# Kernel optimization log

Hardware: AMD Instinct MI355X
Metric: run time of the kernel (lower is better)

Reference implementation:

```python
import jax, jax.numpy as jnp
import numpy as np

EPS = 1e-5


def _interp_conv(x, pos_in, pos_out, idx, w1, b1, w2, b2, kernel, bias):
    # x: [B, Cin, Nin]; idx: [Nout, K] neighbor indices into the input grid.
    off = pos_in[idx] - pos_out[:, None, :]            # [Nout, K, 2] relative offsets
    h = jax.nn.relu(off @ w1 + b1)                     # [Nout, K, 16] weight-net hidden
    A = h @ w2 + b2                                    # [Nout, K, T] interp weights onto T kernel taps
    feat = x[:, :, idx]                                # [B, Cin, Nout, K] irregular gather
    taps = jnp.einsum('bcnk,nkt->bcnt', feat, A)       # resample neighbors onto canonical taps
    return jnp.einsum('bcnt,oct->bon', taps, kernel) + bias[None, :, None]


def _bn_relu(x, g, b):
    # BatchNorm1d (training-style batch stats over (B, N)) + ReLU
    m = x.mean(axis=(0, 2), keepdims=True)
    v = x.var(axis=(0, 2), keepdims=True)
    return jax.nn.relu((x - m) * jax.lax.rsqrt(v + EPS) * g[None, :, None] + b[None, :, None])


def setup_inputs():
    key = jax.random.key(0)
    ks = jax.random.split(key, 24)
    B, N1, N2, N3, K, T = 16, 50176, 12544, 3136, 9, 9
    d = {}
    d['x'] = jax.random.normal(ks[0], (B, 3, N1), jnp.float32)
    d['l1'] = jax.random.uniform(ks[1], (N1, 2), jnp.float32)
    d['l2'] = jax.random.uniform(ks[2], (N2, 2), jnp.float32)
    d['l3'] = jax.random.uniform(ks[3], (N3, 2), jnp.float32)
    d['knn1'] = jax.random.randint(ks[4], (N2, K), 0, N1)
    d['knn2'] = jax.random.randint(ks[5], (N2, K), 0, N2)
    d['knn3'] = jax.random.randint(ks[6], (N2, K), 0, N2)
    d['pool_idx'] = jax.random.randint(ks[7], (N3, 4), 0, N2)
    cins = {'c1': 3, 'c2': 32, 'c3': 32}
    couts = {'c1': 32, 'c2': 32, 'c3': 64}
    for i, p in enumerate(['c1', 'c2', 'c3']):
        d[p + '_wn_w1'] = jax.random.normal(ks[8 + 4 * i], (2, 16), jnp.float32) * 0.5
        d[p + '_wn_b1'] = jnp.zeros(16, jnp.float32)
        d[p + '_wn_w2'] = jax.random.normal(ks[9 + 4 * i], (16, T), jnp.float32) * 0.3
        d[p + '_wn_b2'] = jnp.zeros(T, jnp.float32)
        d[p + '_kernel'] = jax.random.normal(ks[10 + 4 * i], (couts[p], cins[p], T), jnp.float32) * np.float32(1.0 / np.sqrt(cins[p] * T))
        d[p + '_bias'] = jnp.zeros(couts[p], jnp.float32)
    for p, c in [('bn1', 32), ('bn2', 32), ('bn3', 64)]:
        d[p + '_g'] = jnp.ones(c, jnp.float32)
        d[p + '_b'] = jnp.zeros(c, jnp.float32)
    return d


def reference(x, l1, l2, l3, knn1, knn2, knn3, pool_idx,
              c1_wn_w1, c1_wn_b1, c1_wn_w2, c1_wn_b2, c1_kernel, c1_bias,
              c2_wn_w1, c2_wn_b1, c2_wn_w2, c2_wn_b2, c2_kernel, c2_bias,
              c3_wn_w1, c3_wn_b1, c3_wn_w2, c3_wn_b2, c3_kernel, c3_bias,
              bn1_g, bn1_b, bn2_g, bn2_b, bn3_g, bn3_b):
    h = _interp_conv(x, l1, l2, knn1, c1_wn_w1, c1_wn_b1, c1_wn_w2, c1_wn_b2, c1_kernel, c1_bias)
    h = _bn_relu(h, bn1_g, bn1_b)
    h = _interp_conv(h, l2, l2, knn2, c2_wn_w1, c2_wn_b1, c2_wn_w2, c2_wn_b2, c2_kernel, c2_bias)
    h = _bn_relu(h, bn2_g, bn2_b)
    h = _interp_conv(h, l2, l2, knn3, c3_wn_w1, c3_wn_b1, c3_wn_w2, c3_wn_b2, c3_kernel, c3_bias)
    h = _bn_relu(h, bn3_g, bn3_b)
    # MaxPoolNG: max over 4 nearest neighbors on the non-uniform grid -> [B, 64, N3]
    return h[:, :, pool_idx].max(axis=-1)
```

## Files before the change

kernel.cpp:

```cpp
#include <hip/hip_runtime.h>
#include <hip/hip_bf16.h>
#include <cfloat>

#define N1C 50176
#define N2C 12544
#define N3C 3136

typedef __attribute__((ext_vector_type(8))) short short8v;
typedef __attribute__((ext_vector_type(4))) float f32x4;

static __device__ __forceinline__ unsigned short f2bf(float f){
  __hip_bfloat16 h = __float2bfloat16(f);
  return *reinterpret_cast<unsigned short*>(&h);
}
static __device__ __forceinline__ float bflo(unsigned v){
  return __uint_as_float(v << 16);
}
static __device__ __forceinline__ float bfhi(unsigned v){
  return __uint_as_float(v & 0xFFFF0000u);
}
static __device__ __forceinline__ float bf2f(unsigned short u){
  return __uint_as_float(((unsigned)u) << 16);
}
static __device__ __forceinline__ unsigned pk2(float a, float b){
  return (unsigned)f2bf(a) | ((unsigned)f2bf(b) << 16);
}

__global__ __launch_bounds__(256) void transpose_x_kernel(
    const float* __restrict__ x, unsigned short* __restrict__ xTb)
{
  __shared__ float tile[48][65];
  int n0 = blockIdx.x * 64;
  int tid = threadIdx.x;
  int i = tid & 63;
  for (int rr = tid >> 6; rr < 48; rr += 4)
    tile[rr][i] = x[(size_t)rr * N1C + n0 + i];
  __syncthreads();
  for (int j = tid; j < 64*64; j += 256){
    int ii = j >> 6, bc = j & 63, b = bc >> 2, c = bc & 3;
    float v = (c < 3) ? tile[b*3 + c][ii] : 0.f;
    xTb[(size_t)n0 * 64 + j] = f2bf(v);
  }
}

__global__ __launch_bounds__(256) void compute_A_kernel(
    const float* __restrict__ pos_in, const float* __restrict__ pos_out,
    const int* __restrict__ idx,
    const float* __restrict__ w1, const float* __restrict__ b1,
    const float* __restrict__ w2, const float* __restrict__ b2,
    float* __restrict__ Abuf)
{
  int g = blockIdx.x * 256 + threadIdx.x;
  if (g >= N2C * 9) return;
  int n = g / 9;
  int p = idx[g];
  float o0 = pos_in[2*p]   - pos_out[2*n];
  float o1 = pos_in[2*p+1] - pos_out[2*n+1];
  float A[9];
  #pragma unroll
  for (int t = 0; t < 9; t++) A[t] = b2[t];
  #pragma unroll
  for (int j = 0; j < 16; j++){
    float h = fmaxf(fmaf(o0, w1[j], fmaf(o1, w1[16+j], b1[j])), 0.f);
    #pragma unroll
    for (int t = 0; t < 9; t++) A[t] = fmaf(h, w2[j*9 + t], A[t]);
  }
  #pragma unroll
  for (int t = 0; t < 9; t++) Abuf[(size_t)g*9 + t] = A[t];
}

__global__ __launch_bounds__(256) void wcvt_kernel(
    const float* __restrict__ W, unsigned short* __restrict__ Wb,
    int total, int K, int KW, int mode)
{
  int i = blockIdx.x * 256 + threadIdx.x;
  if (i >= total) return;
  int o = i / KW, r = i % KW;
  float v;
  if (mode == 0){
    v = (r < K) ? W[o*K + r] : 0.f;
  } else {
    int t = r >> 5, c = r & 31;
    v = W[o*288 + c*9 + t];
  }
  Wb[i] = f2bf(v);
}

template<int CIN, int CINP, int COUT, int NPB, bool AFFINE>
__global__ __launch_bounds__(256) void conv_mfma_kernel(
    const unsigned short* __restrict__ in, const int* __restrict__ idx,
    const float* __restrict__ Abuf, const unsigned short* __restrict__ Wb,
    const float* __restrict__ bias,
    const float* __restrict__ scale, const float* __restrict__ shift,
    unsigned short* __restrict__ out, float* __restrict__ gpart)
{
  constexpr int K    = CIN * 9;
  constexpr int KW   = (K < 32) ? 32 : K;
  constexpr int KROW = (K < 32) ? 48 : 296;
  constexpr int CHUNKS = KW / 32;
  constexpr int OT   = COUT / 16;
  constexpr int HP   = CINP / 2;
  constexpr int PPT  = 16 * HP;

  __shared__ alignas(16) unsigned short Tb[NPB * 16 * KROW];
  __shared__ float As[NPB * 81];
  __shared__ int   Ip[NPB * 9];
  __shared__ float Sw[4 * COUT];
  __shared__ float Sq[4 * COUT];

  int n0 = blockIdx.x * NPB;
  int tid = threadIdx.x;
  for (int i = tid; i < NPB*81; i += 256) As[i] = Abuf[(size_t)n0*81 + i];
  if (tid < NPB*9) Ip[tid] = idx[n0*9 + tid];
  for (int i = tid; i < 4*COUT; i += 256){ Sw[i] = 0.f; Sq[i] = 0.f; }
  if (K < 32){
    for (int i = tid; i < NPB*16*KROW/2; i += 256) ((unsigned*)Tb)[i] = 0u;
  }
  __syncthreads();

  for (int u = tid; u < NPB*PPT; u += 256){
    int ni = u / PPT, loc = u % PPT;
    int b = loc / HP, c2 = loc % HP;
    const float* As_n = As + ni*81;
    const int*   ip   = Ip + ni*9;
    float scx=1.f, shx=0.f, scy=1.f, shy=0.f;
    if (AFFINE){
      scx = scale[2*c2];   shx = shift[2*c2];
      scy = scale[2*c2+1]; shy = shift[2*c2+1];
    }
    float fx[9], fy[9];
    #pragma unroll
    for (int k = 0; k < 9; k++){
      unsigned v = *(const unsigned*)(in + ((size_t)ip[k]*16 + b)*CINP + 2*c2);
      float x0 = bflo(v), y0 = bfhi(v);
      if (AFFINE){
        x0 = fmaxf(fmaf(x0, scx, shx), 0.f);
        y0 = fmaxf(fmaf(y0, scy, shy), 0.f);
      }
      fx[k] = x0; fy[k] = y0;
    }
    unsigned short e[18];
    #pragma unroll
    for (int t = 0; t < 9; t++){
      float s0 = 0.f, s1 = 0.f;
      #pragma unroll
      for (int k = 0; k < 9; k++){
        float a = As_n[k*9 + t];
        s0 = fmaf(fx[k], a, s0);
        s1 = fmaf(fy[k], a, s1);
      }
      e[t] = f2bf(s0); e[9+t] = f2bf(s1);
    }
    unsigned* dst = (unsigned*)(Tb + (ni*16 + b)*KROW + 18*c2);
    #pragma unroll
    for (int j = 0; j < 9; j++) dst[j] = (unsigned)e[2*j] | ((unsigned)e[2*j+1] << 16);
  }
  __syncthreads();

  int w = tid >> 6, l = tid & 63, lr = l & 15, lg = l >> 4;
  float smr[4] = {0,0,0,0}, sqr[4] = {0,0,0,0};
  int oBase = 0;
  for (int wi = w; wi < NPB*OT; wi += 4){
    int ni = wi / OT, ot = wi % OT;
    oBase = 16*ot + 4*lg;
    f32x4 acc;
    #pragma unroll
    for (int r = 0; r < 4; r++) acc[r] = bias[oBase + r];
    const short8v* ap = (const short8v*)(Wb + (size_t)(16*ot + lr)*KW) + lg;
    const short8v* bp = (const short8v*)(Tb + (ni*16 + lr)*KROW) + lg;
    #pragma unroll
    for (int kk = 0; kk < CHUNKS; kk++)
      acc = __builtin_amdgcn_mfma_f32_16x16x32_bf16(ap[kk*4], bp[kk*4], acc, 0, 0, 0);
    ushort4 o4;
    o4.x = f2bf(acc[0]); o4.y = f2bf(acc[1]); o4.z = f2bf(acc[2]); o4.w = f2bf(acc[3]);
    *(ushort4*)(out + ((size_t)(n0 + ni)*16 + lr)*COUT + oBase) = o4;
    #pragma unroll
    for (int r = 0; r < 4; r++){
      smr[r] += acc[r];
      sqr[r] = fmaf(acc[r], acc[r], sqr[r]);
    }
  }
  #pragma unroll
  for (int m = 1; m < 16; m <<= 1){
    #pragma unroll
    for (int r = 0; r < 4; r++){
      smr[r] += __shfl_xor(smr[r], m);
      sqr[r] += __shfl_xor(sqr[r], m);
    }
  }
  if (lr == 0){
    #pragma unroll
    for (int r = 0; r < 4; r++){
      Sw[w*COUT + oBase + r] = smr[r];
      Sq[w*COUT + oBase + r] = sqr[r];
    }
  }
  __syncthreads();
  for (int o = tid; o < COUT; o += 256){
    float sm = Sw[o] + Sw[COUT + o] + Sw[2*COUT + o] + Sw[3*COUT + o];
    float sq = Sq[o] + Sq[COUT + o] + Sq[2*COUT + o] + Sq[3*COUT + o];
    gpart[(size_t)blockIdx.x * 2*COUT + o] = sm;
    gpart[(size_t)blockIdx.x * 2*COUT + COUT + o] = sq;
  }
}

template<int COUT>
__global__ __launch_bounds__(256, 2) void conv_wave_kernel(
    const unsigned short* __restrict__ in, const int* __restrict__ idx,
    const float* __restrict__ Abuf, const unsigned short* __restrict__ Wb,
    const float* __restrict__ bias,
    const float* __restrict__ scale, const float* __restrict__ shift,
    unsigned short* __restrict__ out, float* __restrict__ gpart)
{
  constexpr int NPB  = 4;
  constexpr int KROW = 296;
  constexpr int OT   = COUT / 16;
  constexpr int AP   = 12;
  constexpr int USZ  = 128;

  __shared__ alignas(16) unsigned short Tb[NPB * 16 * KROW];
  __shared__ alignas(16) float U[NPB * USZ];

  int tid = threadIdx.x;
  int w = tid >> 6, l = tid & 63;
  int n0 = blockIdx.x * NPB;

  int nws = __builtin_amdgcn_readfirstlane(n0 + w);

  const float* Ap = Abuf + (size_t)nws * 81;
  float a0 = Ap[l];
  float a1 = (l < 17) ? Ap[64 + l] : 0.f;

  int ip[9];
  {
    const int* ipr = idx + nws * 9;
    #pragma unroll
    for (int k = 0; k < 9; k++) ip[k] = ipr[k];
  }

  int b = l & 15, cg = l >> 4;
  const unsigned short* gbase = in + b*32 + cg*8;
  uint4 rv[9];
  #pragma unroll
  for (int k = 0; k < 9; k++)
    rv[k] = *(const uint4*)(gbase + (size_t)ip[k]*512);
  float4 scA = *(const float4*)(scale + cg*8);
  float4 scB = *(const float4*)(scale + cg*8 + 4);
  float4 shA = *(const float4*)(shift + cg*8);
  float4 shB = *(const float4*)(shift + cg*8 + 4);
  __builtin_amdgcn_sched_barrier(0);

  float* Aw = U + w * USZ;
  {
    int k = l / 9, t = l - k*9;
    Aw[k*AP + t] = a0;
    if (l < 17){
      int j = l + 64;
      int k2 = j / 9, t2 = j - k2*9;
      Aw[k2*AP + t2] = a1;
    }
  }

  unsigned short* drow = Tb + (size_t)(w*16 + b)*KROW + cg*8;
  #pragma unroll
  for (int h = 0; h < 2; h++){
    f32x4 sc4, sh4;
    if (h == 0){
      sc4[0]=scA.x; sc4[1]=scA.y; sc4[2]=scA.z; sc4[3]=scA.w;
      sh4[0]=shA.x; sh4[1]=shA.y; sh4[2]=shA.z; sh4[3]=shA.w;
    } else {
      sc4[0]=scB.x; sc4[1]=scB.y; sc4[2]=scB.z; sc4[3]=scB.w;
      sh4[0]=shB.x; sh4[1]=shB.y; sh4[2]=shB.z; sh4[3]=shB.w;
    }
    f32x4 tv0={0,0,0,0}, tv1={0,0,0,0}, tv2={0,0,0,0}, tv3={0,0,0,0},
          tv4={0,0,0,0}, tv5={0,0,0,0}, tv6={0,0,0,0}, tv7={0,0,0,0},
          tv8={0,0,0,0};
    #pragma unroll
    for (int k = 0; k < 9; k++){
      unsigned u0 = (h == 0) ? rv[k].x : rv[k].z;
      unsigned u1 = (h == 0) ? rv[k].y : rv[k].w;
      f32x4 f;
      f[0] = bflo(u0); f[1] = bfhi(u0); f[2] = bflo(u1); f[3] = bfhi(u1);
      f = f * sc4 + sh4;
      f[0] = fmaxf(f[0], 0.f); f[1] = fmaxf(f[1], 0.f);
      f[2] = fmaxf(f[2], 0.f); f[3] = fmaxf(f[3], 0.f);
      f32x4 a03 = *(const f32x4*)(Aw + k*AP);
      f32x4 a47 = *(const f32x4*)(Aw + k*AP + 4);
      float a8  = Aw[k*AP + 8];
      tv0 += f * a03[0];
      tv1 += f * a03[1];
      tv2 += f * a03[2];
      tv3 += f * a03[3];
      tv4 += f * a47[0];
      tv5 += f * a47[1];
      tv6 += f * a47[2];
      tv7 += f * a47[3];
      tv8 += f * a8;
    }
    unsigned short* dh = drow + h*4;
    { uint2 o; o.x = pk2(tv0[0],tv0[1]); o.y = pk2(tv0[2],tv0[3]); *(uint2*)(dh + 0*32) = o; }
    { uint2 o; o.x = pk2(tv1[0],tv1[1]); o.y = pk2(tv1[2],tv1[3]); *(uint2*)(dh + 1*32) = o; }
    { uint2 o; o.x = pk2(tv2[0],tv2[1]); o.y = pk2(tv2[2],tv2[3]); *(uint2*)(dh + 2*32) = o; }
    { uint2 o; o.x = pk2(tv3[0],tv3[1]); o.y = pk2(tv3[2],tv3[3]); *(uint2*)(dh + 3*32) = o; }
    { uint2 o; o.x = pk2(tv4[0],tv4[1]); o.y = pk2(tv4[2],tv4[3]); *(uint2*)(dh + 4*32) = o; }
    { uint2 o; o.x = pk2(tv5[0],tv5[1]); o.y = pk2(tv5[2],tv5[3]); *(uint2*)(dh + 5*32) = o; }
    { uint2 o; o.x = pk2(tv6[0],tv6[1]); o.y = pk2(tv6[2],tv6[3]); *(uint2*)(dh + 6*32) = o; }
    { uint2 o; o.x = pk2(tv7[0],tv7[1]); o.y = pk2(tv7[2],tv7[3]); *(uint2*)(dh + 7*32) = o; }
    { uint2 o; o.x = pk2(tv8[0],tv8[1]); o.y = pk2(tv8[2],tv8[3]); *(uint2*)(dh + 8*32) = o; }
  }

  int lr = l & 15, lg = l >> 4;
  const short8v* bp = (const short8v*)(Tb + (size_t)(w*16 + lr)*KROW) + lg;
  #pragma unroll
  for (int ot = 0; ot < OT; ot++){
    int oBase = 16*ot + 4*lg;
    f32x4 a3;
    #pragma unroll
    for (int r = 0; r < 4; r++) a3[r] = bias[oBase + r];
    const short8v* ap = (const short8v*)(Wb + (size_t)(16*ot + lr)*288) + lg;
    #pragma unroll
    for (int kk = 0; kk < 9; kk++)
      a3 = __builtin_amdgcn_mfma_f32_16x16x32_bf16(ap[kk*4], bp[kk*4], a3, 0, 0, 0);
    ushort4 o4;
    o4.x = f2bf(a3[0]); o4.y = f2bf(a3[1]); o4.z = f2bf(a3[2]); o4.w = f2bf(a3[3]);
    *(ushort4*)(out + ((size_t)(n0 + w)*16 + lr)*COUT + oBase) = o4;

    float smr[4], sqr[4];
    #pragma unroll
    for (int r = 0; r < 4; r++){ smr[r] = a3[r]; sqr[r] = a3[r]*a3[r]; }
    #pragma unroll
    for (int m = 1; m < 16; m <<= 1){
      #pragma unroll
      for (int r = 0; r < 4; r++){
        smr[r] += __shfl_xor(smr[r], m);
        sqr[r] += __shfl_xor(sqr[r], m);
      }
    }
    if (lr == 0){
      #pragma unroll
      for (int r = 0; r < 4; r++){
        U[w*USZ + oBase + r]        = smr[r];
        U[w*USZ + COUT + oBase + r] = sqr[r];
      }
    }
  }
  __syncthreads();
  for (int o = tid; o < COUT; o += 256){
    float sm = U[o] + U[USZ + o] + U[2*USZ + o] + U[3*USZ + o];
    float sq = U[COUT + o] + U[USZ + COUT + o] + U[2*USZ + COUT + o] + U[3*USZ + COUT + o];
    gpart[(size_t)blockIdx.x * 2*COUT + o] = sm;
    gpart[(size_t)blockIdx.x * 2*COUT + COUT + o] = sq;
  }
}

__global__ __launch_bounds__(256) void bn_finalize_kernel(
    const float* __restrict__ gpart, int NB, int C,
    const float* __restrict__ g, const float* __restrict__ bb,
    float* __restrict__ sc, float* __restrict__ sh, float invN)
{
  int c = blockIdx.x;
  float sm = 0.f, sq = 0.f;
  for (int i = threadIdx.x; i < NB; i += 256){
    sm += gpart[(size_t)i*2*C + c];
    sq += gpart[(size_t)i*2*C + C + c];
  }
  #pragma unroll
  for (int off = 32; off > 0; off >>= 1){
    sm += __shfl_down(sm, off);
    sq += __shfl_down(sq, off);
  }
  __shared__ float rs[8];
  int wd = threadIdx.x >> 6, ln = threadIdx.x & 63;
  if (ln == 0){ rs[wd] = sm; rs[4+wd] = sq; }
  __syncthreads();
  if (threadIdx.x == 0){
    float S = rs[0]+rs[1]+rs[2]+rs[3], Q = rs[4]+rs[5]+rs[6]+rs[7];
    float mean = S * invN;
    float var  = fmaxf(Q * invN - mean*mean, 0.f);
    float s = g[c] * rsqrtf(var + 1e-5f);
    sc[c] = s;
    sh[c] = bb[c] - mean * s;
  }
}

__global__ __launch_bounds__(256) void pool_kernel(
    const unsigned short* __restrict__ h3, const int* __restrict__ pidx,
    const float* __restrict__ sc, const float* __restrict__ sh,
    float* __restrict__ out)
{
  __shared__ float P[16][1024];
  int m0 = blockIdx.x * 16;
  int tid = threadIdx.x;
  for (int mi = 0; mi < 16; mi++){
    int m = m0 + mi;
    int p0 = pidx[m*4+0], p1 = pidx[m*4+1], p2 = pidx[m*4+2], p3 = pidx[m*4+3];
    #pragma unroll
    for (int q = 0; q < 4; q++){
      int bo = tid + q*256;
      int o = bo & 63;
      float s = sc[o], h = sh[o];
      float v0 = fmaf(bf2f(h3[(size_t)p0*1024 + bo]), s, h);
      float v1 = fmaf(bf2f(h3[(size_t)p1*1024 + bo]), s, h);
      float v2 = fmaf(bf2f(h3[(size_t)p2*1024 + bo]), s, h);
      float v3 = fmaf(bf2f(h3[(size_t)p3*1024 + bo]), s, h);
      P[mi][bo] = fmaxf(fmaxf(fmaxf(v0,v1), fmaxf(v2,v3)), 0.f);
    }
  }
  __syncthreads();
  #pragma unroll
  for (int w = 0; w < 4; w++){
    int r = tid + w*256;
    float* dst = out + (size_t)r*N3C + m0;
    #pragma unroll
    for (int mi = 0; mi < 16; mi++) dst[mi] = P[mi][r];
  }
}

extern "C" void kernel_launch(void* const* d_in, const int* in_sizes, int n_in,
                              void* d_out, int out_size, void* d_ws, size_t ws_size,
                              hipStream_t stream)
{
  const float* x    = (const float*)d_in[0];
  const float* l1   = (const float*)d_in[1];
  const float* l2   = (const float*)d_in[2];
  const int* knn1   = (const int*)d_in[4];
  const int* knn2   = (const int*)d_in[5];
  const int* knn3   = (const int*)d_in[6];
  const int* pidx   = (const int*)d_in[7];

  const float* c1_w1 = (const float*)d_in[8];
  const float* c1_b1 = (const float*)d_in[9];
  const float* c1_w2 = (const float*)d_in[10];
  const float* c1_b2 = (const float*)d_in[11];
  const float* c1_k  = (const float*)d_in[12];
  const float* c1_bs = (const float*)d_in[13];
  const float* c2_w1 = (const float*)d_in[14];
  const float* c2_b1 = (const float*)d_in[15];
  const float* c2_w2 = (const float*)d_in[16];
  const float* c2_b2 = (const float*)d_in[17];
  const float* c2_k  = (const float*)d_in[18];
  const float* c2_bs = (const float*)d_in[19];
  const float* c3_w1 = (const float*)d_in[20];
  const float* c3_b1 = (const float*)d_in[21];
  const float* c3_w2 = (const float*)d_in[22];
  const float* c3_b2 = (const float*)d_in[23];
  const float* c3_k  = (const float*)d_in[24];
  const float* c3_bs = (const float*)d_in[25];
  const float* bn1_g = (const float*)d_in[26];
  const float* bn1_b = (const float*)d_in[27];
  const float* bn2_g = (const float*)d_in[28];
  const float* bn2_b = (const float*)d_in[29];
  const float* bn3_g = (const float*)d_in[30];
  const float* bn3_b = (const float*)d_in[31];

  char* ws = (char*)d_ws;
  unsigned short* xTb = (unsigned short*)(ws + 0);
  unsigned short* h1  = (unsigned short*)(ws + 6422528);
  unsigned short* h2  = (unsigned short*)(ws + 19267584);
  unsigned short* h3  = (unsigned short*)(ws + 32112640);
  float* Abuf         = (float*)(ws + 57802752);
  float* gpart        = (float*)(ws + 61867008);
  unsigned short* wb1 = (unsigned short*)(ws + 65078272);
  unsigned short* wb2 = (unsigned short*)(ws + 65081344);
  unsigned short* wb3 = (unsigned short*)(ws + 65099776);
  float* sc1 = (float*)(ws + 65137664); float* sh1 = sc1 + 32;
  float* sc2 = sh1 + 32;                float* sh2 = sc2 + 32;
  float* sc3 = sh2 + 32;                float* sh3 = sc3 + 64;

  const float invN = 1.0f / (float)(N2C * 16);
  const int ablocks = (N2C * 9 + 255) / 256;

  transpose_x_kernel<<<N1C/64, 256, 0, stream>>>(x, xTb);
  wcvt_kernel<<<(32*32 + 255)/256, 256, 0, stream>>>(c1_k, wb1, 32*32, 27, 32, 0);
  wcvt_kernel<<<(32*288 + 255)/256, 256, 0, stream>>>(c2_k, wb2, 32*288, 288, 288, 1);
  wcvt_kernel<<<(64*288 + 255)/256, 256, 0, stream>>>(c3_k, wb3, 64*288, 288, 288, 1);

  compute_A_kernel<<<ablocks, 256, 0, stream>>>(l1, l2, knn1, c1_w1, c1_b1, c1_w2, c1_b2, Abuf);
  conv_mfma_kernel<3, 4, 32, 8, false><<<N2C/8, 256, 0, stream>>>(
      xTb, knn1, Abuf, wb1, c1_bs, nullptr, nullptr, h1, gpart);
  bn_finalize_kernel<<<32, 256, 0, stream>>>(gpart, N2C/8, 32, bn1_g, bn1_b, sc1, sh1, invN);

  compute_A_kernel<<<ablocks, 256, 0, stream>>>(l2, l2, knn2, c2_w1, c2_b1, c2_w2, c2_b2, Abuf);
  conv_wave_kernel<32><<<N2C/4, 256, 0, stream>>>(
      h1, knn2, Abuf, wb2, c2_bs, sc1, sh1, h2, gpart);
  bn_finalize_kernel<<<32, 256, 0, stream>>>(gpart, N2C/4, 32, bn2_g, bn2_b, sc2, sh2, invN);

  compute_A_kernel<<<ablocks, 256, 0, stream>>>(l2, l2, knn3, c3_w1, c3_b1, c3_w2, c3_b2, Abuf);
  conv_wave_kernel<64><<<N2C/4, 256, 0, stream>>>(
      h2, knn3, Abuf, wb3, c3_bs, sc2, sh2, h3, gpart);
  bn_finalize_kernel<<<64, 256, 0, stream>>>(gpart, N2C/4, 64, bn3_g, bn3_b, sc3, sh3, invN);

  pool_kernel<<<N3C/16, 256, 0, stream>>>(h3, pidx, sc3, sh3, (float*)d_out);
}
```

Measured before the change: 167.4 us.

## Feed MFMA B operands directly from registers, dropping the shared-memory tap staging

The wave-level conv kernel now computes both 4-channel halves of the tap accumulation at once. It packs each tap's 8 bf16 channels straight into a short8v register that matches the MFMA B-fragment layout (lane b = batch row, cg = k-group), so the Tb shared-memory buffer and its write/read round trip go away. The BN statistic reduction across lanes is also deferred until after all output tiles are done. The costs are higher register pressure (18 f32x4 accumulators plus 9 fragments) and a risk of spilling or lower occupancy.

```diff
diff --git a/kernel.cpp b/kernel.cpp
--- a/kernel.cpp
+++ b/kernel.cpp
@@ -24,6 +24,12 @@
 }
 static __device__ __forceinline__ unsigned pk2(float a, float b){
   return (unsigned)f2bf(a) | ((unsigned)f2bf(b) << 16);
+}
+static __device__ __forceinline__ short8v pack8(f32x4 L, f32x4 H){
+  short8v r;
+  r[0]=(short)f2bf(L[0]); r[1]=(short)f2bf(L[1]); r[2]=(short)f2bf(L[2]); r[3]=(short)f2bf(L[3]);
+  r[4]=(short)f2bf(H[0]); r[5]=(short)f2bf(H[1]); r[6]=(short)f2bf(H[2]); r[7]=(short)f2bf(H[3]);
+  return r;
 }
 
 __global__ __launch_bounds__(256) void transpose_x_kernel(
@@ -212,19 +218,15 @@
     const float* __restrict__ scale, const float* __restrict__ shift,
     unsigned short* __restrict__ out, float* __restrict__ gpart)
 {
-  constexpr int NPB  = 4;
-  constexpr int KROW = 296;
-  constexpr int OT   = COUT / 16;
-  constexpr int AP   = 12;
-  constexpr int USZ  = 128;
-
-  __shared__ alignas(16) unsigned short Tb[NPB * 16 * KROW];
+  constexpr int NPB = 4;
+  constexpr int OT  = COUT / 16;
+  constexpr int USZ = 128;
+
   __shared__ alignas(16) float U[NPB * USZ];
 
   int tid = threadIdx.x;
   int w = tid >> 6, l = tid & 63;
   int n0 = blockIdx.x * NPB;
-
   int nws = __builtin_amdgcn_readfirstlane(n0 + w);
 
   const float* Ap = Abuf + (size_t)nws * 81;
@@ -240,116 +242,131 @@
 
   int b = l & 15, cg = l >> 4;
   const unsigned short* gbase = in + b*32 + cg*8;
-  uint4 rv[9];
-  #pragma unroll
-  for (int k = 0; k < 9; k++)
-    rv[k] = *(const uint4*)(gbase + (size_t)ip[k]*512);
-  float4 scA = *(const float4*)(scale + cg*8);
-  float4 scB = *(const float4*)(scale + cg*8 + 4);
-  float4 shA = *(const float4*)(shift + cg*8);
-  float4 shB = *(const float4*)(shift + cg*8 + 4);
+  uint4 rv0 = *(const uint4*)(gbase + (size_t)ip[0]*512);
+  uint4 rv1 = *(const uint4*)(gbase + (size_t)ip[1]*512);
+  uint4 rv2 = *(const uint4*)(gbase + (size_t)ip[2]*512);
+  uint4 rv3 = *(const uint4*)(gbase + (size_t)ip[3]*512);
+  uint4 rv4 = *(const uint4*)(gbase + (size_t)ip[4]*512);
+  uint4 rv5 = *(const uint4*)(gbase + (size_t)ip[5]*512);
+  uint4 rv6 = *(const uint4*)(gbase + (size_t)ip[6]*512);
+  uint4 rv7 = *(const uint4*)(gbase + (size_t)ip[7]*512);
+  uint4 rv8 = *(const uint4*)(gbase + (size_t)ip[8]*512);
+  float4 scLf = *(const float4*)(scale + cg*8);
+  float4 scHf = *(const float4*)(scale + cg*8 + 4);
+  float4 shLf = *(const float4*)(shift + cg*8);
+  float4 shHf = *(const float4*)(shift + cg*8 + 4);
   __builtin_amdgcn_sched_barrier(0);
 
   float* Aw = U + w * USZ;
   {
     int k = l / 9, t = l - k*9;
-    Aw[k*AP + t] = a0;
+    Aw[k*12 + t] = a0;
     if (l < 17){
       int j = l + 64;
       int k2 = j / 9, t2 = j - k2*9;
-      Aw[k2*AP + t2] = a1;
-    }
-  }
-
-  unsigned short* drow = Tb + (size_t)(w*16 + b)*KROW + cg*8;
-  #pragma unroll
-  for (int h = 0; h < 2; h++){
-    f32x4 sc4, sh4;
-    if (h == 0){
-      sc4[0]=scA.x; sc4[1]=scA.y; sc4[2]=scA.z; sc4[3]=scA.w;
-      sh4[0]=shA.x; sh4[1]=shA.y; sh4[2]=shA.z; sh4[3]=shA.w;
-    } else {
-      sc4[0]=scB.x; sc4[1]=scB.y; sc4[2]=scB.z; sc4[3]=scB.w;
-      sh4[0]=shB.x; sh4[1]=shB.y; sh4[2]=shB.z; sh4[3]=shB.w;
-    }
-    f32x4 tv0={0,0,0,0}, tv1={0,0,0,0}, tv2={0,0,0,0}, tv3={0,0,0,0},
-          tv4={0,0,0,0}, tv5={0,0,0,0}, tv6={0,0,0,0}, tv7={0,0,0,0},
-          tv8={0,0,0,0};
-    #pragma unroll
-    for (int k = 0; k < 9; k++){
-      unsigned u0 = (h == 0) ? rv[k].x : rv[k].z;
-      unsigned u1 = (h == 0) ? rv[k].y : rv[k].w;
-      f32x4 f;
-      f[0] = bflo(u0); f[1] = bfhi(u0); f[2] = bflo(u1); f[3] = bfhi(u1);
-      f = f * sc4 + sh4;
-      f[0] = fmaxf(f[0], 0.f); f[1] = fmaxf(f[1], 0.f);
-      f[2] = fmaxf(f[2], 0.f); f[3] = fmaxf(f[3], 0.f);
-      f32x4 a03 = *(const f32x4*)(Aw + k*AP);
-      f32x4 a47 = *(const f32x4*)(Aw + k*AP + 4);
-      float a8  = Aw[k*AP + 8];
-      tv0 += f * a03[0];
-      tv1 += f * a03[1];
-      tv2 += f * a03[2];
-      tv3 += f * a03[3];
-      tv4 += f * a47[0];
-      tv5 += f * a47[1];
-      tv6 += f * a47[2];
-      tv7 += f * a47[3];
-      tv8 += f * a8;
-    }
-    unsigned short* dh = drow + h*4;
-    { uint2 o; o.x = pk2(tv0[0],tv0[1]); o.y = pk2(tv0[2],tv0[3]); *(uint2*)(dh + 0*32) = o; }
-    { uint2 o; o.x = pk2(tv1[0],tv1[1]); o.y = pk2(tv1[2],tv1[3]); *(uint2*)(dh + 1*32) = o; }
-    { uint2 o; o.x = pk2(tv2[0],tv2[1]); o.y = pk2(tv2[2],tv2[3]); *(uint2*)(dh + 2*32) = o; }
-    { uint2 o; o.x = pk2(tv3[0],tv3[1]); o.y = pk2(tv3[2],tv3[3]); *(uint2*)(dh + 3*32) = o; }
-    { uint2 o; o.x = pk2(tv4[0],tv4[1]); o.y = pk2(tv4[2],tv4[3]); *(uint2*)(dh + 4*32) = o; }
-    { uint2 o; o.x = pk2(tv5[0],tv5[1]); o.y = pk2(tv5[2],tv5[3]); *(uint2*)(dh + 5*32) = o; }
-    { uint2 o; o.x = pk2(tv6[0],tv6[1]); o.y = pk2(tv6[2],tv6[3]); *(uint2*)(dh + 6*32) = o; }
-    { uint2 o; o.x = pk2(tv7[0],tv7[1]); o.y = pk2(tv7[2],tv7[3]); *(uint2*)(dh + 7*32) = o; }
-    { uint2 o; o.x = pk2(tv8[0],tv8[1]); o.y = pk2(tv8[2],tv8[3]); *(uint2*)(dh + 8*32) = o; }
-  }
-
-  int lr = l & 15, lg = l >> 4;
-  const short8v* bp = (const short8v*)(Tb + (size_t)(w*16 + lr)*KROW) + lg;
+      Aw[k2*12 + t2] = a1;
+    }
+  }
+
+  f32x4 scL; scL[0]=scLf.x; scL[1]=scLf.y; scL[2]=scLf.z; scL[3]=scLf.w;
+  f32x4 shL; shL[0]=shLf.x; shL[1]=shLf.y; shL[2]=shLf.z; shL[3]=shLf.w;
+  f32x4 scH; scH[0]=scHf.x; scH[1]=scHf.y; scH[2]=scHf.z; scH[3]=scHf.w;
+  f32x4 shH; shH[0]=shHf.x; shH[1]=shHf.y; shH[2]=shHf.z; shH[3]=shHf.w;
+
+  f32x4 tL0={0,0,0,0},tL1={0,0,0,0},tL2={0,0,0,0},tL3={0,0,0,0},tL4={0,0,0,0},
+        tL5={0,0,0,0},tL6={0,0,0,0},tL7={0,0,0,0},tL8={0,0,0,0};
+  f32x4 tH0={0,0,0,0},tH1={0,0,0,0},tH2={0,0,0,0},tH3={0,0,0,0},tH4={0,0,0,0},
+        tH5={0,0,0,0},tH6={0,0,0,0},tH7={0,0,0,0},tH8={0,0,0,0};
+
+#define KSTEP(RV, K) { \
+    f32x4 fL_, fH_; \
+    fL_[0]=bflo(RV.x); fL_[1]=bfhi(RV.x); fL_[2]=bflo(RV.y); fL_[3]=bfhi(RV.y); \
+    fH_[0]=bflo(RV.z); fH_[1]=bfhi(RV.z); fH_[2]=bflo(RV.w); fH_[3]=bfhi(RV.w); \
+    fL_ = fL_ * scL + shL; fH_ = fH_ * scH + shH; \
+    fL_[0]=fmaxf(fL_[0],0.f); fL_[1]=fmaxf(fL_[1],0.f); \
+    fL_[2]=fmaxf(fL_[2],0.f); fL_[3]=fmaxf(fL_[3],0.f); \
+    fH_[0]=fmaxf(fH_[0],0.f); fH_[1]=fmaxf(fH_[1],0.f); \
+    fH_[2]=fmaxf(fH_[2],0.f); fH_[3]=fmaxf(fH_[3],0.f); \
+    f32x4 a03_ = *(const f32x4*)(Aw + (K)*12); \
+    f32x4 a47_ = *(const f32x4*)(Aw + (K)*12 + 4); \
+    float a8_ = Aw[(K)*12 + 8]; \
+    tL0 += fL_ * a03_[0]; tH0 += fH_ * a03_[0]; \
+    tL1 += fL_ * a03_[1]; tH1 += fH_ * a03_[1]; \
+    tL2 += fL_ * a03_[2]; tH2 += fH_ * a03_[2]; \
+    tL3 += fL_ * a03_[3]; tH3 += fH_ * a03_[3]; \
+    tL4 += fL_ * a47_[0]; tH4 += fH_ * a47_[0]; \
+    tL5 += fL_ * a47_[1]; tH5 += fH_ * a47_[1]; \
+    tL6 += fL_ * a47_[2]; tH6 += fH_ * a47_[2]; \
+    tL7 += fL_ * a47_[3]; tH7 += fH_ * a47_[3]; \
+    tL8 += fL_ * a8_;     tH8 += fH_ * a8_; }
+
+  KSTEP(rv0,0) KSTEP(rv1,1) KSTEP(rv2,2) KSTEP(rv3,3) KSTEP(rv4,4)
+  KSTEP(rv5,5) KSTEP(rv6,6) KSTEP(rv7,7) KSTEP(rv8,8)
+#undef KSTEP
+
+  short8v fr0 = pack8(tL0, tH0);
+  short8v fr1 = pack8(tL1, tH1);
+  short8v fr2 = pack8(tL2, tH2);
+  short8v fr3 = pack8(tL3, tH3);
+  short8v fr4 = pack8(tL4, tH4);
+  short8v fr5 = pack8(tL5, tH5);
+  short8v fr6 = pack8(tL6, tH6);
+  short8v fr7 = pack8(tL7, tH7);
+  short8v fr8 = pack8(tL8, tH8);
+
+  f32x4 sm0={0,0,0,0}, sm1={0,0,0,0}, sm2={0,0,0,0}, sm3={0,0,0,0};
+  f32x4 sq0={0,0,0,0}, sq1={0,0,0,0}, sq2={0,0,0,0}, sq3={0,0,0,0};
   #pragma unroll
   for (int ot = 0; ot < OT; ot++){
-    int oBase = 16*ot + 4*lg;
+    int oBase = 16*ot + 4*cg;
     f32x4 a3;
-    #pragma unroll
-    for (int r = 0; r < 4; r++) a3[r] = bias[oBase + r];
-    const short8v* ap = (const short8v*)(Wb + (size_t)(16*ot + lr)*288) + lg;
-    #pragma unroll
-    for (int kk = 0; kk < 9; kk++)
-      a3 = __builtin_amdgcn_mfma_f32_16x16x32_bf16(ap[kk*4], bp[kk*4], a3, 0, 0, 0);
+    a3[0]=bias[oBase]; a3[1]=bias[oBase+1]; a3[2]=bias[oBase+2]; a3[3]=bias[oBase+3];
+    const short8v* ap = (const short8v*)(Wb + (size_t)(16*ot + b)*288) + cg;
+    a3 = __builtin_amdgcn_mfma_f32_16x16x32_bf16(ap[0],  fr0, a3, 0, 0, 0);
+    a3 = __builtin_amdgcn_mfma_f32_16x16x32_bf16(ap[4],  fr1, a3, 0, 0, 0);
+    a3 = __builtin_amdgcn_mfma_f32_16x16x32_bf16(ap[8],  fr2, a3, 0, 0, 0);
+    a3 = __builtin_amdgcn_mfma_f32_16x16x32_bf16(ap[12], fr3, a3, 0, 0, 0);
+    a3 = __builtin_amdgcn_mfma_f32_16x16x32_bf16(ap[16], fr4, a3, 0, 0, 0);
+    a3 = __builtin_amdgcn_mfma_f32_16x16x32_bf16(ap[20], fr5, a3, 0, 0, 0);
+    a3 = __builtin_amdgcn_mfma_f32_16x16x32_bf16(ap[24], fr6, a3, 0, 0, 0);
+    a3 = __builtin_amdgcn_mfma_f32_16x16x32_bf16(ap[28], fr7, a3, 0, 0, 0);
+    a3 = __builtin_amdgcn_mfma_f32_16x16x32_bf16(ap[32], fr8, a3, 0, 0, 0);
     ushort4 o4;
     o4.x = f2bf(a3[0]); o4.y = f2bf(a3[1]); o4.z = f2bf(a3[2]); o4.w = f2bf(a3[3]);
-    *(ushort4*)(out + ((size_t)(n0 + w)*16 + lr)*COUT + oBase) = o4;
-
-    float smr[4], sqr[4];
-    #pragma unroll
-    for (int r = 0; r < 4; r++){ smr[r] = a3[r]; sqr[r] = a3[r]*a3[r]; }
+    *(ushort4*)(out + ((size_t)nws*16 + b)*COUT + oBase) = o4;
+    if (ot==0){ sm0 += a3; sq0 += a3*a3; }
+    else if (ot==1){ sm1 += a3; sq1 += a3*a3; }
+    else if (ot==2){ sm2 += a3; sq2 += a3*a3; }
+    else { sm3 += a3; sq3 += a3*a3; }
+  }
+
+  #pragma unroll
+  for (int ot = 0; ot < OT; ot++){
+    f32x4 s = (ot==0) ? sm0 : ((ot==1) ? sm1 : ((ot==2) ? sm2 : sm3));
+    f32x4 q = (ot==0) ? sq0 : ((ot==1) ? sq1 : ((ot==2) ? sq2 : sq3));
     #pragma unroll
     for (int m = 1; m < 16; m <<= 1){
       #pragma unroll
       for (int r = 0; r < 4; r++){
-        smr[r] += __shfl_xor(smr[r], m);
-        sqr[r] += __shfl_xor(sqr[r], m);
+        s[r] += __shfl_xor(s[r], m);
+        q[r] += __shfl_xor(q[r], m);
       }
     }
-    if (lr == 0){
+    if (b == 0){
+      int oBase = 16*ot + 4*cg;
       #pragma unroll
       for (int r = 0; r < 4; r++){
-        U[w*USZ + oBase + r]        = smr[r];
-        U[w*USZ + COUT + oBase + r] = sqr[r];
+        U[w*USZ + oBase + r]        = s[r];
+        U[w*USZ + COUT + oBase + r] = q[r];
       }
     }
   }
   __syncthreads();
   for (int o = tid; o < COUT; o += 256){
-    float sm = U[o] + U[USZ + o] + U[2*USZ + o] + U[3*USZ + o];
-    float sq = U[COUT + o] + U[USZ + COUT + o] + U[2*USZ + COUT + o] + U[3*USZ + COUT + o];
-    gpart[(size_t)blockIdx.x * 2*COUT + o] = sm;
-    gpart[(size_t)blockIdx.x * 2*COUT + COUT + o] = sq;
+    float smv = U[o] + U[USZ + o] + U[2*USZ + o] + U[3*USZ + o];
+    float sqv = U[COUT + o] + U[USZ + COUT + o] + U[2*USZ + COUT + o] + U[3*USZ + COUT + o];
+    gpart[(size_t)blockIdx.x * 2*COUT + o] = smv;
+    gpart[(size_t)blockIdx.x * 2*COUT + COUT + o] = sqv;
   }
 }
 
```

Measured after the change: 171.1 us. 2.2% more time.
